# Optimization experiments

Hardware: AMD Instinct MI355X
Metric: run time of the kernel (lower is better)

Reference implementation:

```python
import jax, jax.numpy as jnp
import numpy as np

N = 50000      # nodes
E = 800000     # edges (avg degree 16)
F_IN = 32
H = 64         # hidden_features
E_DIM = 16     # edge_dim
C_OUT = 40
L = 2          # num_layers
G = 64         # graphs in batch
BN_EPS = 1e-5
GEN_EPS = 1e-7  # PyG GENConv message eps


def setup_inputs() -> dict:
    key = jax.random.key(0)
    ks = jax.random.split(key, 12)
    s = 0.05
    inp = {}
    inp["x"] = jax.random.normal(ks[0], (N, F_IN), jnp.float32)
    inp["edge_index"] = jax.random.randint(ks[1], (2, E), 0, N)
    inp["edge_attr"] = jax.random.normal(ks[2], (E, E_DIM), jnp.float32)
    inp["batch"] = jnp.sort(jax.random.randint(ks[3], (N,), 0, G))
    # input linear
    inp["lin_in_w"] = jax.random.normal(ks[4], (F_IN, H), jnp.float32) * s
    inp["lin_in_b"] = jnp.zeros((H,), jnp.float32)
    # per-layer DeepGCNLayer norm (BatchNorm affine)
    inp["norm_gamma"] = jnp.ones((L, H), jnp.float32)
    inp["norm_beta"] = jnp.zeros((L, H), jnp.float32)
    # per-layer GENConv params
    inp["edge_w"] = jax.random.normal(ks[5], (L, E_DIM, H), jnp.float32) * s
    inp["edge_b"] = jnp.zeros((L, H), jnp.float32)
    inp["t"] = jnp.ones((L,), jnp.float32)  # learned softmax temperature
    inp["mlp_w1"] = jax.random.normal(ks[6], (L, H, 2 * H), jnp.float32) * s
    inp["mlp_b1"] = jnp.zeros((L, 2 * H), jnp.float32)
    inp["mlp_gamma"] = jnp.ones((L, 2 * H), jnp.float32)
    inp["mlp_beta"] = jnp.zeros((L, 2 * H), jnp.float32)
    inp["mlp_w2"] = jax.random.normal(ks[7], (L, 2 * H, H), jnp.float32) * s
    inp["mlp_b2"] = jnp.zeros((L, H), jnp.float32)
    # output linear
    inp["lin_out_w"] = jax.random.normal(ks[8], (H, C_OUT), jnp.float32) * s
    inp["lin_out_b"] = jnp.zeros((C_OUT,), jnp.float32)
    return inp


def _batch_norm(x, gamma, beta):
    mu = jnp.mean(x, axis=0)
    var = jnp.var(x, axis=0)
    return (x - mu) * jax.lax.rsqrt(var + BN_EPS) * gamma + beta


def _gen_conv(x, src, dst, e_emb, t, w1, b1, g1, be1, w2, b2):
    # message: relu(x_j + edge_emb) + eps   -> [E, H]
    m = jax.nn.relu(x[src] + e_emb) + GEN_EPS
    # softmax aggregation over destination neighborhoods with temperature t
    logits = m * t
    seg_max = jax.ops.segment_max(logits, dst, num_segments=N)      # [N, H]
    ex = jnp.exp(logits - seg_max[dst])                              # [E, H]
    denom = jax.ops.segment_sum(ex, dst, num_segments=N)            # [N, H]
    agg = jax.ops.segment_sum(ex * m, dst, num_segments=N) / (denom + 1e-16)
    # root add, then GENConv MLP: Linear(H,2H) -> BN -> ReLU -> Linear(2H,H)
    out = agg + x
    h = out @ w1 + b1
    h = jax.nn.relu(_batch_norm(h, g1, be1))
    return h @ w2 + b2


def reference(x, edge_index, edge_attr, batch, lin_in_w, lin_in_b,
              norm_gamma, norm_beta, edge_w, edge_b, t,
              mlp_w1, mlp_b1, mlp_gamma, mlp_beta, mlp_w2, mlp_b2,
              lin_out_w, lin_out_b):
    src, dst = edge_index[0], edge_index[1]
    h = x @ lin_in_w + lin_in_b                                      # [N, H]
    for l in range(L):
        # DeepGCNLayer res+ : norm -> act -> (dropout p=0) -> conv, residual add
        z = jax.nn.relu(_batch_norm(h, norm_gamma[l], norm_beta[l]))
        e_emb = edge_attr @ edge_w[l] + edge_b[l]                    # [E, H]
        c = _gen_conv(z, src, dst, e_emb, t[l], mlp_w1[l], mlp_b1[l],
                      mlp_gamma[l], mlp_beta[l], mlp_w2[l], mlp_b2[l])
        h = h + c
    # global mean pool per graph
    sums = jax.ops.segment_sum(h, batch, num_segments=G)             # [G, H]
    counts = jax.ops.segment_sum(jnp.ones((N, 1), h.dtype), batch, num_segments=G)
    pooled = sums / jnp.maximum(counts, 1.0)
    out = jax.nn.relu(pooled) @ lin_out_w + lin_out_b                # [G, C_OUT]
    return out
```

## Files before the change

kernel.cpp:

```cpp
#include <hip/hip_runtime.h>

#define N_NODES 50000
#define N_EDGES 800000
#define F_INP   32
#define HDIM    64
#define EDIM    16
#define COUT    40
#define NGRAPH  64
#define LDS_STRIDE 18
#define CPAD    16

typedef float v2f __attribute__((ext_vector_type(2)));

__global__ void hist_kernel(const int* __restrict__ dst, int* __restrict__ cnt, int E) {
    int base = (blockIdx.x * 256 + threadIdx.x) * 4;
    if (base >= E) return;
    int4 d4 = *(const int4*)(dst + base);
    atomicAdd(&cnt[(size_t)d4.x * CPAD], 1);
    atomicAdd(&cnt[(size_t)d4.y * CPAD], 1);
    atomicAdd(&cnt[(size_t)d4.z * CPAD], 1);
    atomicAdd(&cnt[(size_t)d4.w * CPAD], 1);
}

__global__ void scan_part_kernel(const int* __restrict__ cnt, int* __restrict__ bsum, int n) {
    __shared__ int red[256];
    int tid = threadIdx.x;
    int idx = blockIdx.x * 256 + tid;
    red[tid] = (idx < n) ? cnt[(size_t)idx * CPAD] : 0;
    __syncthreads();
    for (int off = 128; off > 0; off >>= 1) {
        if (tid < off) red[tid] += red[tid + off];
        __syncthreads();
    }
    if (tid == 0) bsum[blockIdx.x] = red[0];
}

__global__ void scan_top_kernel(int* __restrict__ bsum, int nb) {
    __shared__ int tmp[256];
    int tid = threadIdx.x;
    int v = (tid < nb) ? bsum[tid] : 0;
    tmp[tid] = v;
    __syncthreads();
    for (int off = 1; off < 256; off <<= 1) {
        int x = (tid >= off) ? tmp[tid - off] : 0;
        __syncthreads();
        tmp[tid] += x;
        __syncthreads();
    }
    if (tid < nb) bsum[tid] = tmp[tid] - v;
}

__global__ void scan_apply_kernel(const int* __restrict__ cnt, const int* __restrict__ bsum,
                                  int* __restrict__ cursor, int n) {
    __shared__ int tmp[256];
    int tid = threadIdx.x;
    int idx = blockIdx.x * 256 + tid;
    int v = (idx < n) ? cnt[(size_t)idx * CPAD] : 0;
    tmp[tid] = v;
    __syncthreads();
    for (int off = 1; off < 256; off <<= 1) {
        int x = (tid >= off) ? tmp[tid - off] : 0;
        __syncthreads();
        tmp[tid] += x;
        __syncthreads();
    }
    int excl = tmp[tid] - v + bsum[blockIdx.x];
    if (idx < n) cursor[(size_t)idx * CPAD] = excl;
}

__global__ void scatter_kernel(const int* __restrict__ dst, const int* __restrict__ src,
                               int* __restrict__ cursor, int4* __restrict__ edge4, int E) {
    int base = (blockIdx.x * 256 + threadIdx.x) * 4;
    if (base >= E) return;
    int4 d4 = *(const int4*)(dst + base);
    int4 s4 = *(const int4*)(src + base);
    int p0 = atomicAdd(&cursor[(size_t)d4.x * CPAD], 1);
    int p1 = atomicAdd(&cursor[(size_t)d4.y * CPAD], 1);
    int p2 = atomicAdd(&cursor[(size_t)d4.z * CPAD], 1);
    int p3 = atomicAdd(&cursor[(size_t)d4.w * CPAD], 1);
    edge4[p0] = make_int4(d4.x, s4.x, base + 0, 0);
    edge4[p1] = make_int4(d4.y, s4.y, base + 1, 0);
    edge4[p2] = make_int4(d4.z, s4.z, base + 2, 0);
    edge4[p3] = make_int4(d4.w, s4.w, base + 3, 0);
}

__global__ void gstart_kernel(const int* __restrict__ batch, int* __restrict__ gstart,
                              int N, int G) {
    int n = blockIdx.x * 256 + threadIdx.x;
    if (n >= N) return;
    int g  = batch[n];
    int gp = (n == 0) ? -1 : batch[n - 1];
    for (int gg = gp + 1; gg <= g; gg++) gstart[gg] = n;
    if (n == N - 1) {
        for (int gg = g + 1; gg <= G; gg++) gstart[gg] = N;
    }
}

__global__ void lin_in_kernel(const float* __restrict__ x, const float* __restrict__ W,
                              const float* __restrict__ b, float* __restrict__ h, int N) {
    int tid = threadIdx.x;
    int c = tid & 63;
    float w[F_INP];
#pragma unroll
    for (int k = 0; k < F_INP; k++) w[k] = W[k * HDIM + c];
    int node = blockIdx.x * 4 + (tid >> 6);
    if (node >= N) return;
    const float4* xr = (const float4*)(x + (size_t)node * F_INP);
    float acc = b[c];
#pragma unroll
    for (int k4 = 0; k4 < F_INP / 4; k4++) {
        float4 xv = xr[k4];
        acc += xv.x * w[k4 * 4 + 0] + xv.y * w[k4 * 4 + 1]
             + xv.z * w[k4 * 4 + 2] + xv.w * w[k4 * 4 + 3];
    }
    h[(size_t)node * HDIM + c] = acc;
}

template <int C>
__global__ void bn_stats_kernel(const float* __restrict__ x, float* __restrict__ stats, int N) {
    const int RPB = 256 / C;
    int tid = threadIdx.x;
    int c = tid % C;
    int row0 = blockIdx.x * RPB + tid / C;
    int stride = gridDim.x * RPB;
    float s = 0.f, ss = 0.f;
    for (int r = row0; r < N; r += stride) {
        float v = x[(size_t)r * C + c];
        s += v; ss += v * v;
    }
    __shared__ float ls[256], lss[256];
    ls[tid] = s; lss[tid] = ss;
    __syncthreads();
    if (tid < C) {
        for (int k = 1; k < RPB; k++) { s += ls[tid + k * C]; ss += lss[tid + k * C]; }
        atomicAdd(&stats[c], s);
        atomicAdd(&stats[C + c], ss);
    }
}

__global__ __launch_bounds__(256) void edge_agg_kernel(
        const float* __restrict__ h, const float* __restrict__ ea,
        const int4* __restrict__ edge4,
        const float* __restrict__ We, const float* __restrict__ be,
        const float* __restrict__ tptr, const float* __restrict__ stats,
        const float* __restrict__ gamma, const float* __restrict__ beta,
        float* __restrict__ num, float* __restrict__ den) {
    __shared__ float sA[4 * 64 * LDS_STRIDE];
    int tid = threadIdx.x;
    int c  = tid & 63;
    int wv = tid >> 6;
    float inv = 1.0f / (float)N_NODES;
    float mu  = stats[c] * inv;
    float var = stats[HDIM + c] * inv - mu * mu;
    float sc  = rsqrtf(var + 1e-5f) * gamma[c];
    float sb  = beta[c] - mu * sc;
    v2f w2[8];
#pragma unroll
    for (int k = 0; k < 8; k++) {
        w2[k].x = We[(2 * k) * HDIM + c];
        w2[k].y = We[(2 * k + 1) * HDIM + c];
    }
    float bc = be[c];
    float tl2 = (*tptr) * 1.4426950408889634f;

    int p = (blockIdx.x * 4 + wv) * 64 + c;
    int4 pk = edge4[p];
    int d_own = pk.x;
    int s_own = pk.y;
    int e     = pk.z;
    float* myrow = &sA[(wv * 64 + c) * LDS_STRIDE];
    {
        const float4* ar = (const float4*)(ea + (size_t)e * EDIM);
        float4 a0 = ar[0], a1 = ar[1], a2 = ar[2], a3 = ar[3];
        myrow[0]=a0.x;  myrow[1]=a0.y;  myrow[2]=a0.z;  myrow[3]=a0.w;
        myrow[4]=a1.x;  myrow[5]=a1.y;  myrow[6]=a1.z;  myrow[7]=a1.w;
        myrow[8]=a2.x;  myrow[9]=a2.y;  myrow[10]=a2.z; myrow[11]=a2.w;
        myrow[12]=a3.x; myrow[13]=a3.y; myrow[14]=a3.z; myrow[15]=a3.w;
    }
    int dprev = __shfl_up(d_own, 1);
    unsigned long long bmask = __ballot(c > 0 && d_own != dprev);
    __syncthreads();

    const float* wrow = &sA[(size_t)wv * 64 * LDS_STRIDE];
    float nacc = 0.f, dacc = 0.f;
    int cur_d = __builtin_amdgcn_readlane(d_own, 0);
#pragma unroll 1
    for (int jj = 0; jj < 64; jj += 8) {
        float hv[8];
#pragma unroll
        for (int u = 0; u < 8; u++) {
            int su = __builtin_amdgcn_readlane(s_own, jj + u);
            hv[u] = h[(size_t)su * HDIM + c];
        }
#pragma unroll
        for (int u = 0; u < 8; u++) {
            if (bmask & (1ull << (jj + u))) {
                atomicAdd(&num[(size_t)cur_d * HDIM + c], nacc);
                atomicAdd(&den[(size_t)cur_d * HDIM + c], dacc);
                nacc = 0.f; dacc = 0.f;
                cur_d = __builtin_amdgcn_readlane(d_own, jj + u);
            }
            const v2f* arow = (const v2f*)&wrow[(jj + u) * LDS_STRIDE];
            v2f acc2 = {bc, 0.f};
#pragma unroll
            for (int k2 = 0; k2 < 8; k2++)
                acc2 += arow[k2] * w2[k2];
            float acc = acc2.x + acc2.y;
            float zv = fmaxf(hv[u] * sc + sb, 0.f);
            float m  = fmaxf(zv + acc, 0.f) + 1e-7f;
            float ex = exp2f(m * tl2);
            dacc += ex;
            nacc += ex * m;
        }
    }
    atomicAdd(&num[(size_t)cur_d * HDIM + c], nacc);
    atomicAdd(&den[(size_t)cur_d * HDIM + c], dacc);
}

__global__ __launch_bounds__(256) void mlp1_kernel(
        float* __restrict__ num, float* __restrict__ den,
        const float* __restrict__ h, const float* __restrict__ stats,
        const float* __restrict__ gamma, const float* __restrict__ beta,
        const float* __restrict__ W1, const float* __restrict__ b1,
        float* __restrict__ h1, int N) {
    __shared__ float sW[HDIM * 128];
    __shared__ float srow[32 * 65];
    int tid = threadIdx.x;
    for (int i = tid; i < HDIM * 128; i += 256) sW[i] = W1[i];
    int base = blockIdx.x * 32;
    {
        int cc = tid & 63;
        float inv = 1.0f / (float)N_NODES;
        float mu  = stats[cc] * inv;
        float var = stats[HDIM + cc] * inv - mu * mu;
        float rs  = rsqrtf(var + 1e-5f);
        float ga  = gamma[cc], bb = beta[cc];
        for (int i = tid; i < 32 * HDIM; i += 256) {
            int r = i >> 6;
            int node = base + r;
            float v = 0.f;
            if (node < N) {
                size_t idx = (size_t)node * HDIM + cc;
                float hv = h[idx];
                float z  = fmaxf((hv - mu) * rs * ga + bb, 0.f);
                float nu = num[idx], de = den[idx];
                num[idx] = 0.f; den[idx] = 0.f;
                v = nu / (de + 1e-16f) + z;
            }
            srow[r * 65 + cc] = v;
        }
    }
    __syncthreads();
    int tx = tid & 31;
    int ty = tid >> 5;
    float acc[4][4];
    float b0 = b1[4 * tx], bb1 = b1[4 * tx + 1], b2v = b1[4 * tx + 2], b3 = b1[4 * tx + 3];
#pragma unroll
    for (int j = 0; j < 4; j++) { acc[j][0] = b0; acc[j][1] = bb1; acc[j][2] = b2v; acc[j][3] = b3; }
#pragma unroll 8
    for (int k = 0; k < HDIM; k++) {
        float4 wv = *(const float4*)&sW[k * 128 + 4 * tx];
        float r0 = srow[(ty * 4 + 0) * 65 + k];
        float r1 = srow[(ty * 4 + 1) * 65 + k];
        float r2 = srow[(ty * 4 + 2) * 65 + k];
        float r3 = srow[(ty * 4 + 3) * 65 + k];
        acc[0][0] += r0 * wv.x; acc[0][1] += r0 * wv.y; acc[0][2] += r0 * wv.z; acc[0][3] += r0 * wv.w;
        acc[1][0] += r1 * wv.x; acc[1][1] += r1 * wv.y; acc[1][2] += r1 * wv.z; acc[1][3] += r1 * wv.w;
        acc[2][0] += r2 * wv.x; acc[2][1] += r2 * wv.y; acc[2][2] += r2 * wv.z; acc[2][3] += r2 * wv.w;
        acc[3][0] += r3 * wv.x; acc[3][1] += r3 * wv.y; acc[3][2] += r3 * wv.z; acc[3][3] += r3 * wv.w;
    }
#pragma unroll
    for (int j = 0; j < 4; j++) {
        int node = base + ty * 4 + j;
        if (node < N)
            *(float4*)&h1[(size_t)node * 128 + 4 * tx] =
                make_float4(acc[j][0], acc[j][1], acc[j][2], acc[j][3]);
    }
}

__global__ __launch_bounds__(256) void mlp2_kernel(
        const float* __restrict__ h1, const float* __restrict__ stats,
        const float* __restrict__ mg, const float* __restrict__ mb,
        const float* __restrict__ W2, const float* __restrict__ b2,
        float* __restrict__ h, int N) {
    __shared__ float sW[128 * HDIM];
    __shared__ float sact[32 * 129];
    __shared__ float sbn[4 * 128];
    int tid = threadIdx.x;
    for (int i = tid; i < 128 * HDIM; i += 256) sW[i] = W2[i];
    if (tid < 128) {
        float inv = 1.0f / (float)N;
        float mu  = stats[tid] * inv;
        float var = stats[128 + tid] * inv - mu * mu;
        sbn[tid]       = mu;
        sbn[128 + tid] = rsqrtf(var + 1e-5f);
        sbn[256 + tid] = mg[tid];
        sbn[384 + tid] = mb[tid];
    }
    __syncthreads();
    int base = blockIdx.x * 32;
    for (int i = tid; i < 32 * 128; i += 256) {
        int r = i >> 7, o = i & 127;
        int node = base + r;
        float v = 0.f;
        if (node < N) {
            v = h1[(size_t)node * 128 + o];
            v = fmaxf((v - sbn[o]) * sbn[128 + o] * sbn[256 + o] + sbn[384 + o], 0.f);
        }
        sact[r * 129 + o] = v;
    }
    __syncthreads();
    int tx = tid & 15;
    int ty = tid >> 4;
    float acc[2][4];
    float b0 = b2[4 * tx], bb1 = b2[4 * tx + 1], b2v = b2[4 * tx + 2], b3 = b2[4 * tx + 3];
    acc[0][0] = b0; acc[0][1] = bb1; acc[0][2] = b2v; acc[0][3] = b3;
    acc[1][0] = b0; acc[1][1] = bb1; acc[1][2] = b2v; acc[1][3] = b3;
#pragma unroll 8
    for (int k = 0; k < 128; k++) {
        float4 wv = *(const float4*)&sW[k * HDIM + 4 * tx];
        float r0 = sact[(ty * 2 + 0) * 129 + k];
        float r1 = sact[(ty * 2 + 1) * 129 + k];
        acc[0][0] += r0 * wv.x; acc[0][1] += r0 * wv.y; acc[0][2] += r0 * wv.z; acc[0][3] += r0 * wv.w;
        acc[1][0] += r1 * wv.x; acc[1][1] += r1 * wv.y; acc[1][2] += r1 * wv.z; acc[1][3] += r1 * wv.w;
    }
#pragma unroll
    for (int j = 0; j < 2; j++) {
        int node = base + ty * 2 + j;
        if (node < N) {
            float4* p = (float4*)&h[(size_t)node * HDIM + 4 * tx];
            float4 old = *p;
            *p = make_float4(old.x + acc[j][0], old.y + acc[j][1],
                             old.z + acc[j][2], old.w + acc[j][3]);
        }
    }
}

__global__ void pool_out_kernel(const float* __restrict__ h, const int* __restrict__ gstart,
                                const float* __restrict__ Wo, const float* __restrict__ bo,
                                float* __restrict__ out, int N) {
    __shared__ float sp[HDIM];
    __shared__ float red[256];
    __shared__ float sW[HDIM * COUT];
    int g = blockIdx.x;
    int tid = threadIdx.x;
    for (int i = tid; i < HDIM * COUT; i += 256) sW[i] = Wo[i];
    int beg = gstart[g], end = gstart[g + 1];
    int c = tid & 63, r0 = tid >> 6;
    float s0 = 0.f, s1 = 0.f, s2 = 0.f, s3 = 0.f;
    int r = beg + r0;
    for (; r + 12 < end; r += 16) {
        s0 += h[(size_t)(r     ) * HDIM + c];
        s1 += h[(size_t)(r +  4) * HDIM + c];
        s2 += h[(size_t)(r +  8) * HDIM + c];
        s3 += h[(size_t)(r + 12) * HDIM + c];
    }
    for (; r < end; r += 4) s0 += h[(size_t)r * HDIM + c];
    red[tid] = (s0 + s1) + (s2 + s3);
    __syncthreads();
    if (tid < HDIM) {
        float s = red[tid] + red[tid + 64] + red[tid + 128] + red[tid + 192];
        float cnt = (float)(end - beg);
        float pooled = s / fmaxf(cnt, 1.0f);
        sp[tid] = fmaxf(pooled, 0.0f);
    }
    __syncthreads();
    if (tid < COUT) {
        float acc = bo[tid];
#pragma unroll
        for (int k = 0; k < HDIM; k++) acc += sp[k] * sW[k * COUT + tid];
        out[g * COUT + tid] = acc;
    }
}

extern "C" void kernel_launch(void* const* d_in, const int* in_sizes, int n_in,
                              void* d_out, int out_size, void* d_ws, size_t ws_size,
                              hipStream_t stream) {
    (void)in_sizes; (void)n_in; (void)out_size; (void)ws_size;
    const float* x          = (const float*)d_in[0];
    const int*   eidx       = (const int*)  d_in[1];
    const float* eattr      = (const float*)d_in[2];
    const int*   batch      = (const int*)  d_in[3];
    const float* lin_in_w   = (const float*)d_in[4];
    const float* lin_in_b   = (const float*)d_in[5];
    const float* norm_gamma = (const float*)d_in[6];
    const float* norm_beta  = (const float*)d_in[7];
    const float* edge_w     = (const float*)d_in[8];
    const float* edge_b     = (const float*)d_in[9];
    const float* tparam     = (const float*)d_in[10];
    const float* mlp_w1     = (const float*)d_in[11];
    const float* mlp_b1     = (const float*)d_in[12];
    const float* mlp_gamma  = (const float*)d_in[13];
    const float* mlp_beta   = (const float*)d_in[14];
    const float* mlp_w2     = (const float*)d_in[15];
    const float* mlp_b2     = (const float*)d_in[16];
    const float* lin_out_w  = (const float*)d_in[17];
    const float* lin_out_b  = (const float*)d_in[18];
    float* out = (float*)d_out;

    const int* src = eidx;
    const int* dst = eidx + N_EDGES;

    char* ws = (char*)d_ws;
    size_t off = 0;
    auto alloc = [&](size_t bytes) -> char* {
        char* p = ws + off;
        off = (off + bytes + 255) & ~(size_t)255;
        return p;
    };
    float* statsA0 = (float*)alloc(128 * 4);
    float* statsB0 = (float*)alloc(256 * 4);
    float* statsA1 = (float*)alloc(128 * 4);
    float* statsB1 = (float*)alloc(256 * 4);
    size_t zero_bytes = off;
    int*   bsum    = (int*)  alloc(256 * 4);
    int4*  edge4   = (int4*) alloc((size_t)N_EDGES * 16);
    int*   gstart  = (int*)  alloc((size_t)(NGRAPH + 1) * 4);
    float* h       = (float*)alloc((size_t)N_NODES * HDIM * 4);
    float* num     = (float*)alloc((size_t)N_NODES * HDIM * 4);
    float* den     = (float*)alloc((size_t)N_NODES * HDIM * 4);
    float* h1      = (float*)alloc((size_t)N_NODES * 2 * HDIM * 4);
    int*   cnt     = (int*)h1;
    int*   cursor  = (int*)((char*)h1 + (size_t)N_NODES * CPAD * 4);

    hipMemsetAsync(d_ws, 0, zero_bytes, stream);
    hipMemsetAsync(cnt, 0, (size_t)N_NODES * CPAD * 4, stream);
    hipMemsetAsync(num, 0, (size_t)N_NODES * HDIM * 4 * 2, stream);

    const int NB = (N_NODES + 255) / 256;
    const int EB4 = (N_EDGES / 4 + 255) / 256;
    hist_kernel      <<<EB4, 256, 0, stream>>>(dst, cnt, N_EDGES);
    scan_part_kernel <<<NB, 256, 0, stream>>>(cnt, bsum, N_NODES);
    scan_top_kernel  <<<1, 256, 0, stream>>>(bsum, NB);
    scan_apply_kernel<<<NB, 256, 0, stream>>>(cnt, bsum, cursor, N_NODES);
    scatter_kernel   <<<EB4, 256, 0, stream>>>(dst, src, cursor, edge4, N_EDGES);
    gstart_kernel    <<<NB, 256, 0, stream>>>(batch, gstart, N_NODES, NGRAPH);
    lin_in_kernel    <<<(N_NODES + 3) / 4, 256, 0, stream>>>(x, lin_in_w, lin_in_b, h, N_NODES);

    const int AGG_BLOCKS = N_EDGES / 256;

    float* statsA[2] = { statsA0, statsA1 };
    float* statsB[2] = { statsB0, statsB1 };
    for (int l = 0; l < 2; l++) {
        bn_stats_kernel<64><<<256, 256, 0, stream>>>(h, statsA[l], N_NODES);
        edge_agg_kernel<<<AGG_BLOCKS, 256, 0, stream>>>(
            h, eattr, edge4,
            edge_w + (size_t)l * EDIM * HDIM, edge_b + l * HDIM,
            tparam + l, statsA[l], norm_gamma + l * HDIM, norm_beta + l * HDIM,
            num, den);
        mlp1_kernel<<<(N_NODES + 31) / 32, 256, 0, stream>>>(
            num, den, h, statsA[l], norm_gamma + l * HDIM, norm_beta + l * HDIM,
            mlp_w1 + (size_t)l * HDIM * 2 * HDIM, mlp_b1 + l * 2 * HDIM, h1, N_NODES);
        bn_stats_kernel<128><<<256, 256, 0, stream>>>(h1, statsB[l], N_NODES);
        mlp2_kernel<<<(N_NODES + 31) / 32, 256, 0, stream>>>(
            h1, statsB[l], mlp_gamma + l * 2 * HDIM, mlp_beta + l * 2 * HDIM,
            mlp_w2 + (size_t)l * 2 * HDIM * HDIM, mlp_b2 + l * HDIM, h, N_NODES);
    }
    pool_out_kernel<<<NGRAPH, 256, 0, stream>>>(h, gstart, lin_out_w, lin_out_b, out, N_NODES);
}
```

Before: 592.0 us.

## Merge preprocessing kernels and fold scan top level into apply

```diff
diff --git a/kernel.cpp b/kernel.cpp
--- a/kernel.cpp
+++ b/kernel.cpp
@@ -10,16 +10,53 @@
 #define LDS_STRIDE 18
 #define CPAD    16
 
+#define HIST_B  782
+#define NB_B    196
+#define LIN_B   12500
+
 typedef float v2f __attribute__((ext_vector_type(2)));
 
-__global__ void hist_kernel(const int* __restrict__ dst, int* __restrict__ cnt, int E) {
-    int base = (blockIdx.x * 256 + threadIdx.x) * 4;
-    if (base >= E) return;
-    int4 d4 = *(const int4*)(dst + base);
-    atomicAdd(&cnt[(size_t)d4.x * CPAD], 1);
-    atomicAdd(&cnt[(size_t)d4.y * CPAD], 1);
-    atomicAdd(&cnt[(size_t)d4.z * CPAD], 1);
-    atomicAdd(&cnt[(size_t)d4.w * CPAD], 1);
+__global__ __launch_bounds__(256) void prep_kernel(
+        const int* __restrict__ dst, int* __restrict__ cnt,
+        const int* __restrict__ batch, int* __restrict__ gstart,
+        const float* __restrict__ x, const float* __restrict__ W,
+        const float* __restrict__ b, float* __restrict__ h) {
+    int bid = blockIdx.x;
+    int tid = threadIdx.x;
+    if (bid < HIST_B) {
+        int base = (bid * 256 + tid) * 4;
+        if (base >= N_EDGES) return;
+        int4 d4 = *(const int4*)(dst + base);
+        atomicAdd(&cnt[(size_t)d4.x * CPAD], 1);
+        atomicAdd(&cnt[(size_t)d4.y * CPAD], 1);
+        atomicAdd(&cnt[(size_t)d4.z * CPAD], 1);
+        atomicAdd(&cnt[(size_t)d4.w * CPAD], 1);
+    } else if (bid < HIST_B + NB_B) {
+        int n = (bid - HIST_B) * 256 + tid;
+        if (n >= N_NODES) return;
+        int g  = batch[n];
+        int gp = (n == 0) ? -1 : batch[n - 1];
+        for (int gg = gp + 1; gg <= g; gg++) gstart[gg] = n;
+        if (n == N_NODES - 1) {
+            for (int gg = g + 1; gg <= NGRAPH; gg++) gstart[gg] = N_NODES;
+        }
+    } else {
+        int c = tid & 63;
+        float w[F_INP];
+#pragma unroll
+        for (int k = 0; k < F_INP; k++) w[k] = W[k * HDIM + c];
+        int node = (bid - HIST_B - NB_B) * 4 + (tid >> 6);
+        if (node >= N_NODES) return;
+        const float4* xr = (const float4*)(x + (size_t)node * F_INP);
+        float acc = b[c];
+#pragma unroll
+        for (int k4 = 0; k4 < F_INP / 4; k4++) {
+            float4 xv = xr[k4];
+            acc += xv.x * w[k4 * 4 + 0] + xv.y * w[k4 * 4 + 1]
+                 + xv.z * w[k4 * 4 + 2] + xv.w * w[k4 * 4 + 3];
+        }
+        h[(size_t)node * HDIM + c] = acc;
+    }
 }
 
 __global__ void scan_part_kernel(const int* __restrict__ cnt, int* __restrict__ bsum, int n) {
@@ -35,10 +72,22 @@
     if (tid == 0) bsum[blockIdx.x] = red[0];
 }
 
-__global__ void scan_top_kernel(int* __restrict__ bsum, int nb) {
+__global__ void scan_apply_kernel(const int* __restrict__ cnt, const int* __restrict__ bsum,
+                                  int* __restrict__ cursor, int n) {
     __shared__ int tmp[256];
-    int tid = threadIdx.x;
-    int v = (tid < nb) ? bsum[tid] : 0;
+    __shared__ int rb[256];
+    int tid = threadIdx.x;
+    int bb = 0;
+    for (int j = tid; j < blockIdx.x; j += 256) bb += bsum[j];
+    rb[tid] = bb;
+    __syncthreads();
+    for (int off = 128; off > 0; off >>= 1) {
+        if (tid < off) rb[tid] += rb[tid + off];
+        __syncthreads();
+    }
+    int base = rb[0];
+    int idx = blockIdx.x * 256 + tid;
+    int v = (idx < n) ? cnt[(size_t)idx * CPAD] : 0;
     tmp[tid] = v;
     __syncthreads();
     for (int off = 1; off < 256; off <<= 1) {
@@ -47,73 +96,48 @@
         tmp[tid] += x;
         __syncthreads();
     }
-    if (tid < nb) bsum[tid] = tmp[tid] - v;
-}
-
-__global__ void scan_apply_kernel(const int* __restrict__ cnt, const int* __restrict__ bsum,
-                                  int* __restrict__ cursor, int n) {
-    __shared__ int tmp[256];
-    int tid = threadIdx.x;
-    int idx = blockIdx.x * 256 + tid;
-    int v = (idx < n) ? cnt[(size_t)idx * CPAD] : 0;
-    tmp[tid] = v;
-    __syncthreads();
-    for (int off = 1; off < 256; off <<= 1) {
-        int x = (tid >= off) ? tmp[tid - off] : 0;
+    int excl = tmp[tid] - v + base;
+    if (idx < n) cursor[(size_t)idx * CPAD] = excl;
+}
+
+__global__ __launch_bounds__(256) void scatter_bn_kernel(
+        const int* __restrict__ dst, const int* __restrict__ src,
+        int* __restrict__ cursor, int4* __restrict__ edge4,
+        const float* __restrict__ h, float* __restrict__ stats) {
+    __shared__ float ls[256], lss[256];
+    int bid = blockIdx.x;
+    int tid = threadIdx.x;
+    if (bid < HIST_B) {
+        int base = (bid * 256 + tid) * 4;
+        if (base >= N_EDGES) return;
+        int4 d4 = *(const int4*)(dst + base);
+        int4 s4 = *(const int4*)(src + base);
+        int p0 = atomicAdd(&cursor[(size_t)d4.x * CPAD], 1);
+        int p1 = atomicAdd(&cursor[(size_t)d4.y * CPAD], 1);
+        int p2 = atomicAdd(&cursor[(size_t)d4.z * CPAD], 1);
+        int p3 = atomicAdd(&cursor[(size_t)d4.w * CPAD], 1);
+        edge4[p0] = make_int4(d4.x, s4.x, base + 0, 0);
+        edge4[p1] = make_int4(d4.y, s4.y, base + 1, 0);
+        edge4[p2] = make_int4(d4.z, s4.z, base + 2, 0);
+        edge4[p3] = make_int4(d4.w, s4.w, base + 3, 0);
+    } else {
+        int vb = bid - HIST_B;
+        int c = tid & 63;
+        int row0 = vb * 4 + (tid >> 6);
+        float s = 0.f, ss = 0.f;
+        for (int r = row0; r < N_NODES; r += 1024) {
+            float v = h[(size_t)r * HDIM + c];
+            s += v; ss += v * v;
+        }
+        ls[tid] = s; lss[tid] = ss;
         __syncthreads();
-        tmp[tid] += x;
-        __syncthreads();
-    }
-    int excl = tmp[tid] - v + bsum[blockIdx.x];
-    if (idx < n) cursor[(size_t)idx * CPAD] = excl;
-}
-
-__global__ void scatter_kernel(const int* __restrict__ dst, const int* __restrict__ src,
-                               int* __restrict__ cursor, int4* __restrict__ edge4, int E) {
-    int base = (blockIdx.x * 256 + threadIdx.x) * 4;
-    if (base >= E) return;
-    int4 d4 = *(const int4*)(dst + base);
-    int4 s4 = *(const int4*)(src + base);
-    int p0 = atomicAdd(&cursor[(size_t)d4.x * CPAD], 1);
-    int p1 = atomicAdd(&cursor[(size_t)d4.y * CPAD], 1);
-    int p2 = atomicAdd(&cursor[(size_t)d4.z * CPAD], 1);
-    int p3 = atomicAdd(&cursor[(size_t)d4.w * CPAD], 1);
-    edge4[p0] = make_int4(d4.x, s4.x, base + 0, 0);
-    edge4[p1] = make_int4(d4.y, s4.y, base + 1, 0);
-    edge4[p2] = make_int4(d4.z, s4.z, base + 2, 0);
-    edge4[p3] = make_int4(d4.w, s4.w, base + 3, 0);
-}
-
-__global__ void gstart_kernel(const int* __restrict__ batch, int* __restrict__ gstart,
-                              int N, int G) {
-    int n = blockIdx.x * 256 + threadIdx.x;
-    if (n >= N) return;
-    int g  = batch[n];
-    int gp = (n == 0) ? -1 : batch[n - 1];
-    for (int gg = gp + 1; gg <= g; gg++) gstart[gg] = n;
-    if (n == N - 1) {
-        for (int gg = g + 1; gg <= G; gg++) gstart[gg] = N;
-    }
-}
-
-__global__ void lin_in_kernel(const float* __restrict__ x, const float* __restrict__ W,
-                              const float* __restrict__ b, float* __restrict__ h, int N) {
-    int tid = threadIdx.x;
-    int c = tid & 63;
-    float w[F_INP];
-#pragma unroll
-    for (int k = 0; k < F_INP; k++) w[k] = W[k * HDIM + c];
-    int node = blockIdx.x * 4 + (tid >> 6);
-    if (node >= N) return;
-    const float4* xr = (const float4*)(x + (size_t)node * F_INP);
-    float acc = b[c];
-#pragma unroll
-    for (int k4 = 0; k4 < F_INP / 4; k4++) {
-        float4 xv = xr[k4];
-        acc += xv.x * w[k4 * 4 + 0] + xv.y * w[k4 * 4 + 1]
-             + xv.z * w[k4 * 4 + 2] + xv.w * w[k4 * 4 + 3];
-    }
-    h[(size_t)node * HDIM + c] = acc;
+        if (tid < 64) {
+            float ts  = ls[tid] + ls[tid + 64] + ls[tid + 128] + ls[tid + 192];
+            float tss = lss[tid] + lss[tid + 64] + lss[tid + 128] + lss[tid + 192];
+            atomicAdd(&stats[c], ts);
+            atomicAdd(&stats[HDIM + c], tss);
+        }
+    }
 }
 
 template <int C>
@@ -427,22 +451,20 @@
     hipMemsetAsync(cnt, 0, (size_t)N_NODES * CPAD * 4, stream);
     hipMemsetAsync(num, 0, (size_t)N_NODES * HDIM * 4 * 2, stream);
 
-    const int NB = (N_NODES + 255) / 256;
-    const int EB4 = (N_EDGES / 4 + 255) / 256;
-    hist_kernel      <<<EB4, 256, 0, stream>>>(dst, cnt, N_EDGES);
-    scan_part_kernel <<<NB, 256, 0, stream>>>(cnt, bsum, N_NODES);
-    scan_top_kernel  <<<1, 256, 0, stream>>>(bsum, NB);
-    scan_apply_kernel<<<NB, 256, 0, stream>>>(cnt, bsum, cursor, N_NODES);
-    scatter_kernel   <<<EB4, 256, 0, stream>>>(dst, src, cursor, edge4, N_EDGES);
-    gstart_kernel    <<<NB, 256, 0, stream>>>(batch, gstart, N_NODES, NGRAPH);
-    lin_in_kernel    <<<(N_NODES + 3) / 4, 256, 0, stream>>>(x, lin_in_w, lin_in_b, h, N_NODES);
+    prep_kernel      <<<HIST_B + NB_B + LIN_B, 256, 0, stream>>>(
+        dst, cnt, batch, gstart, x, lin_in_w, lin_in_b, h);
+    scan_part_kernel <<<NB_B, 256, 0, stream>>>(cnt, bsum, N_NODES);
+    scan_apply_kernel<<<NB_B, 256, 0, stream>>>(cnt, bsum, cursor, N_NODES);
+    scatter_bn_kernel<<<HIST_B + 256, 256, 0, stream>>>(
+        dst, src, cursor, edge4, h, statsA0);
 
     const int AGG_BLOCKS = N_EDGES / 256;
 
     float* statsA[2] = { statsA0, statsA1 };
     float* statsB[2] = { statsB0, statsB1 };
     for (int l = 0; l < 2; l++) {
-        bn_stats_kernel<64><<<256, 256, 0, stream>>>(h, statsA[l], N_NODES);
+        if (l == 1)
+            bn_stats_kernel<64><<<256, 256, 0, stream>>>(h, statsA1, N_NODES);
         edge_agg_kernel<<<AGG_BLOCKS, 256, 0, stream>>>(
             h, eattr, edge4,
             edge_w + (size_t)l * EDIM * HDIM, edge_b + l * HDIM,
```

New measurement: 580.8 us. Within noise of the previous version (-1.9%).
